# Kernel tuning notes

Measured on AMD Instinct MI355X. Metric: run time of the kernel, lower is better.

Reference implementation:

```python
import jax, jax.numpy as jnp
import numpy as np
from jax import lax

EPS = 1e-5

def conv2d(x, w, b=None, stride=1, pad=1):
    y = lax.conv_general_dilated(x, w, (stride, stride), ((pad, pad), (pad, pad)),
                                 dimension_numbers=('NCHW', 'OIHW', 'NCHW'))
    if b is not None:
        y = y + b[None, :, None, None]
    return y

def dcn(x, w_off, b_off, w, b):
    # modulated deformable conv (DCNv2): k=3, stride=1, pad=1, deformable_groups=1
    B, C, H, W = x.shape
    K = 9
    om = conv2d(x, w_off, b_off)  # [B, 3K, H, W] -> y-offsets, x-offsets, mask logits
    off_y, off_x = om[:, :K], om[:, K:2 * K]
    mask = jax.nn.sigmoid(om[:, 2 * K:])
    ky, kx = jnp.meshgrid(jnp.arange(3) - 1, jnp.arange(3) - 1, indexing='ij')
    py = jnp.arange(H)[None, None, :, None] + ky.reshape(K)[None, :, None, None] + off_y  # [B,K,H,W]
    px = jnp.arange(W)[None, None, None, :] + kx.reshape(K)[None, :, None, None] + off_x
    x_flat = x.reshape(B, C, H * W)
    y0 = jnp.floor(py)
    x0 = jnp.floor(px)
    acc = jnp.zeros((B, C, K, H * W), x.dtype)
    for dy in (0.0, 1.0):  # 4 bilinear corners (fixed small loop)
        for dx in (0.0, 1.0):
            yi = y0 + dy
            xi = x0 + dx
            wgt = (1.0 - jnp.abs(py - yi)) * (1.0 - jnp.abs(px - xi))
            valid = (yi >= 0) & (yi < H) & (xi >= 0) & (xi < W)  # zero padding outside
            yc = jnp.clip(yi, 0, H - 1).astype(jnp.int32)
            xc = jnp.clip(xi, 0, W - 1).astype(jnp.int32)
            flat = (yc * W + xc).reshape(B, K, H * W)
            g = jnp.take_along_axis(x_flat[:, :, None, :], flat[:, None, :, :], axis=3)  # [B,C,K,HW]
            acc = acc + g * (wgt * valid).reshape(B, 1, K, H * W)
    acc = acc * mask.reshape(B, 1, K, H * W)
    out = jnp.einsum('bckp,ock->bop', acc, w.reshape(w.shape[0], C, K))
    return out.reshape(B, w.shape[0], H, W) + b[None, :, None, None]

def bn_relu(x, gamma, beta, mean, var):
    inv = gamma / jnp.sqrt(var + EPS)
    return jax.nn.relu(x * inv[None, :, None, None] + (beta - mean * inv)[None, :, None, None])

def up_depthwise(x, w_up, f):
    # ConvTranspose2d(o, o, 2f, stride=f, padding=f//2, groups=o, bias=False)
    k = 2 * f
    p = k - 1 - f // 2
    return lax.conv_general_dilated(x, w_up[:, :, ::-1, ::-1], (1, 1), ((p, p), (p, p)),
                                    lhs_dilation=(f, f),
                                    dimension_numbers=('NCHW', 'OIHW', 'NCHW'),
                                    feature_group_count=w_up.shape[0])

def setup_inputs():
    key = jax.random.key(0)
    ks = jax.random.split(key, 12)
    B, CI, CO, H, W = 4, 256, 128, 64, 64
    f32 = jnp.float32
    d = {}
    d['x'] = jax.random.normal(ks[0], (B, CI, H, W), f32)
    d['w_off1'] = jax.random.normal(ks[1], (27, CI, 3, 3), f32) * 0.01
    d['b_off1'] = jnp.zeros((27,), f32)
    d['w1'] = jax.random.normal(ks[2], (CO, CI, 3, 3), f32) * (1.0 / np.sqrt(CI * 9))
    d['b1'] = jnp.zeros((CO,), f32)
    d['g1'] = jnp.ones((CO,), f32)
    d['be1'] = jnp.zeros((CO,), f32)
    d['m1'] = jax.random.normal(ks[3], (CO,), f32) * 0.1
    d['v1'] = jax.random.uniform(ks[4], (CO,), f32, 0.5, 1.5)
    d['w_up'] = jax.random.normal(ks[5], (CO, 1, 4, 4), f32) * 0.25
    d['w_off2'] = jax.random.normal(ks[6], (27, CO, 3, 3), f32) * 0.01
    d['b_off2'] = jnp.zeros((27,), f32)
    d['w2'] = jax.random.normal(ks[7], (CO, CO, 3, 3), f32) * (1.0 / np.sqrt(CO * 9))
    d['b2'] = jnp.zeros((CO,), f32)
    d['g2'] = jnp.ones((CO,), f32)
    d['be2'] = jnp.zeros((CO,), f32)
    d['m2'] = jax.random.normal(ks[8], (CO,), f32) * 0.1
    d['v2'] = jax.random.uniform(ks[9], (CO,), f32, 0.5, 1.5)
    return d

def reference(x, w_off1, b_off1, w1, b1, g1, be1, m1, v1, w_up,
              w_off2, b_off2, w2, b2, g2, be2, m2, v2):
    y = bn_relu(dcn(x, w_off1, b_off1, w1, b1), g1, be1, m1, v1)   # proj: [B,128,64,64]
    y = up_depthwise(y, w_up, 2)                                    # up:   [B,128,128,128]
    y = bn_relu(dcn(y, w_off2, b_off2, w2, b2), g2, be2, m2, v2)   # node: [B,128,128,128]
    return y
```

## Files before the change

### kernel.cpp

```cpp
#include <hip/hip_runtime.h>
#include <hip/hip_bf16.h>
#include <cmath>


#define EPSV 1e-5f

typedef __attribute__((ext_vector_type(8))) short short8;
typedef __attribute__((ext_vector_type(4))) float f32x4;

__device__ __forceinline__ ushort f2bf(float f) {
    union { float f; uint u; } v; v.f = f;
    const uint r = v.u + 0x7fffu + ((v.u >> 16) & 1u);
    return (ushort)(r >> 16);
}
__device__ __forceinline__ float bf2f(ushort h) {
    union { uint u; float f; } v; v.u = ((uint)h) << 16;
    return v.f;
}
__device__ __forceinline__ float2 ld2u(const float* p) {
    float2 v; __builtin_memcpy(&v, p, sizeof(float2)); return v;
}
__device__ __forceinline__ uint cvtpk_bf16(float a, float b) {
    uint r;
    asm("v_cvt_pk_bf16_f32 %0, %1, %2" : "=v"(r) : "v"(a), "v"(b));
    return r;
}

template <int KS>
__device__ __forceinline__ void pack_store8(
    const float* s, ushort* __restrict__ Shi, ushort* __restrict__ Slo,
    int pp, int j0)
{
    uint hw[4], lw[4];
#pragma unroll
    for (int q = 0; q < 4; ++q) {
        const float s0 = s[2 * q], s1 = s[2 * q + 1];
        const uint h = cvtpk_bf16(s0, s1);
        union { uint u; float f; } h0, h1;
        h0.u = h << 16;
        h1.u = h & 0xffff0000u;
        hw[q] = h;
        lw[q] = cvtpk_bf16(s0 - h0.f, s1 - h1.f);
    }
    uint4 hv; hv.x = hw[0]; hv.y = hw[1]; hv.z = hw[2]; hv.w = hw[3];
    uint4 lv; lv.x = lw[0]; lv.y = lw[1]; lv.z = lw[2]; lv.w = lw[3];
    *(uint4*)&Shi[pp * KS + j0] = hv;
    *(uint4*)&Slo[pp * KS + j0] = lv;
}

__global__ __launch_bounds__(256) void wsplit_perm_kernel(
    const float* __restrict__ w, ushort* __restrict__ hi,
    ushort* __restrict__ lo, int cin, int n)
{
    const int i = blockIdx.x * 256 + threadIdx.x;
    if (i >= n) return;
    const int cin9 = cin * 9;
    const int co = i / cin9;
    const int k  = i - co * cin9;
    const int ch = k >> 5;
    const int kq = (k & 31) >> 3;
    const int j  = k & 7;
    const int mt = co >> 4;
    const int lane = (co & 15) | (kq << 4);
    const size_t dst = ((size_t)(ch * 8 + mt) * 64 + lane) * 8 + j;
    const float f = w[i];
    const ushort h = f2bf(f);
    hi[dst] = h;
    lo[dst] = f2bf(f - bf2f(h));
}

__global__ __launch_bounds__(256) void wsplit_perm_conv_kernel(
    const float* __restrict__ w, ushort* __restrict__ hi,
    ushort* __restrict__ lo, int cin, int n)
{
    const int i = blockIdx.x * 256 + threadIdx.x;
    if (i >= n) return;
    const int cin9 = cin * 9;
    const int co = i / cin9;
    const int k  = i - co * cin9;
    const int ch = k >> 5;
    const int kq = (k & 31) >> 3;
    const int j  = k & 7;
    const int mt = co >> 4;
    const int lane = (co & 15) | (kq << 4);
    const size_t dst = ((size_t)(ch * 2 + mt) * 64 + lane) * 8 + j;
    const float f = (co < 27) ? w[(size_t)co * cin9 + k] : 0.f;
    const ushort h = f2bf(f);
    hi[dst] = h;
    lo[dst] = f2bf(f - bf2f(h));
}

template <int CIN, int HH, int WW, int POS, int KS>
__device__ __forceinline__ void conv_sample_chunk(
    const float* __restrict__ xb, const uint* __restrict__ toff,
    const float* __restrict__ twt, ushort* __restrict__ Shi,
    ushort* __restrict__ Slo, int tt, int kbase)
{
    constexpr int HW = HH * WW;
    const int pp = tt & (POS - 1);
    const int j0 = (tt / POS) * 8;
    float s[8];
#pragma unroll
    for (int j = 0; j < 8; ++j) {
        const int kg = kbase + j0 + j;
        const int c  = (kg * 7282) >> 16;
        const int k9 = kg - c * 9;
        const int ei = k9 * POS + pp;
        s[j] = xb[(size_t)c * HW + toff[ei]] * twt[ei];
    }
    pack_store8<KS>(s, Shi, Slo, pp, j0);
}

template <int CIN, int HH, int WW, int POS, int KWAVES, int MINW>
__global__ __launch_bounds__((POS / 16) * KWAVES * 64, MINW) void conv_mfma_kernel(
    const float* __restrict__ in,
    const ushort* __restrict__ whi,
    const ushort* __restrict__ wlo,
    const float* __restrict__ bias,
    float* __restrict__ om)
{
    constexpr int HW   = HH * WW;
    constexpr int K    = CIN * 9;
    constexpr int NPQ  = POS / 16;
    constexpr int NT   = NPQ * KWAVES * 64;
    constexpr int KC   = 32;
    constexpr int KS   = 40;
    constexpr int NCHT = K / KC;
    constexpr int NCH  = NCHT / KWAVES;
    constexpr int SBUF = POS * KS;

    extern __shared__ __align__(16) char smem[];
    uint*   toff  = (uint*)smem;
    float*  twt   = (float*)(toff + 9 * POS);
    ushort* Sbase = (ushort*)(twt + 9 * POS);

    const int tid = threadIdx.x;
    const int nt  = HW / POS;
    const int cpx = gridDim.x >> 3;
    const int bid = (blockIdx.x & 7) * cpx + (blockIdx.x >> 3);
    const int b   = bid / nt;
    const int p0  = (bid - b * nt) * POS;

    for (int i = tid; i < 9 * POS; i += NT) {
        const int k9 = i / POS, pp = i - k9 * POS;
        const int p  = p0 + pp;
        const int yy = p / WW, xx = p - yy * WW;
        const int ky = (k9 * 11) >> 5, kx = k9 - ky * 3;
        const int iy = yy + ky - 1, ix = xx + kx - 1;
        const bool v = (iy >= 0) && (iy < HH) && (ix >= 0) && (ix < WW);
        const int cy = min(max(iy, 0), HH - 1);
        const int cx = min(max(ix, 0), WW - 1);
        toff[i] = (uint)(cy * WW + cx);
        twt[i]  = v ? 1.f : 0.f;
    }
    __syncthreads();

    const float* xb = in + (size_t)b * CIN * HW;
    const int lane = tid & 63;
    const int w    = tid >> 6;
    const int wq   = w & (NPQ - 1);
    const int kgid = w / NPQ;
    const int tt   = tid & (NPQ * 64 - 1);
    ushort* S00 = Sbase + kgid * (4 * SBUF);

    f32x4 acc[2];
    acc[0] = (f32x4){0.f, 0.f, 0.f, 0.f};
    acc[1] = (f32x4){0.f, 0.f, 0.f, 0.f};
    const int mrow = lane & 15;
    const int kq   = lane >> 4;

    conv_sample_chunk<CIN, HH, WW, POS, KS>(xb, toff, twt, S00, S00 + SBUF,
                                            tt, kgid * NCH * KC);
    __syncthreads();

    for (int ch = 0; ch < NCH; ++ch) {
        const int cur = ch & 1;
        ushort* Sc = S00 + (cur * 2) * SBUF;
        const int boff = (wq * 16 + mrow) * KS + kq * 8;
        const short8 bh = *(const short8*)&Sc[boff];
        const short8 bl = *(const short8*)&Sc[SBUF + boff];
        if (ch + 1 < NCH) {
            ushort* Sn = S00 + ((cur ^ 1) * 2) * SBUF;
            conv_sample_chunk<CIN, HH, WW, POS, KS>(xb, toff, twt,
                                                    Sn, Sn + SBUF, tt,
                                                    (kgid * NCH + ch + 1) * KC);
        }
        const size_t abase = (size_t)((kgid * NCH + ch) * 2) * 512;
        __builtin_amdgcn_s_setprio(1);
#pragma unroll
        for (int mt = 0; mt < 2; ++mt) {
            const size_t ao = abase + (size_t)((mt * 64 + lane) * 8);
            const short8 ah = *(const short8*)(whi + ao);
            const short8 al = *(const short8*)(wlo + ao);
            acc[mt] = __builtin_amdgcn_mfma_f32_16x16x32_bf16(al, bh, acc[mt], 0, 0, 0);
            acc[mt] = __builtin_amdgcn_mfma_f32_16x16x32_bf16(ah, bl, acc[mt], 0, 0, 0);
            acc[mt] = __builtin_amdgcn_mfma_f32_16x16x32_bf16(ah, bh, acc[mt], 0, 0, 0);
        }
        __builtin_amdgcn_s_setprio(0);
        __syncthreads();
    }

    const int pcolb = wq * 16 + mrow;
    constexpr int RS = POS + 1;
    constexpr int SL = 32 * RS;
    float* red = (float*)Sbase;

    if constexpr (KWAVES == 4) {
        if (kgid >= 2) {
#pragma unroll
            for (int mt = 0; mt < 2; ++mt)
#pragma unroll
                for (int r = 0; r < 4; ++r) {
                    const int co = mt * 16 + kq * 4 + r;
                    red[(kgid - 2) * SL + co * RS + pcolb] = acc[mt][r];
                }
        }
        __syncthreads();
        if (kgid < 2) {
#pragma unroll
            for (int mt = 0; mt < 2; ++mt)
#pragma unroll
                for (int r = 0; r < 4; ++r) {
                    const int co = mt * 16 + kq * 4 + r;
                    acc[mt][r] += red[kgid * SL + co * RS + pcolb];
                }
        }
        __syncthreads();
        if (kgid == 1) {
#pragma unroll
            for (int mt = 0; mt < 2; ++mt)
#pragma unroll
                for (int r = 0; r < 4; ++r) {
                    const int co = mt * 16 + kq * 4 + r;
                    red[co * RS + pcolb] = acc[mt][r];
                }
        }
        __syncthreads();
        if (kgid == 0) {
#pragma unroll
            for (int mt = 0; mt < 2; ++mt)
#pragma unroll
                for (int r = 0; r < 4; ++r) {
                    const int co = mt * 16 + kq * 4 + r;
                    acc[mt][r] += red[co * RS + pcolb];
                }
        }
    } else if constexpr (KWAVES == 2) {
        if (kgid == 1) {
#pragma unroll
            for (int mt = 0; mt < 2; ++mt)
#pragma unroll
                for (int r = 0; r < 4; ++r) {
                    const int co = mt * 16 + kq * 4 + r;
                    red[co * RS + pcolb] = acc[mt][r];
                }
        }
        __syncthreads();
        if (kgid == 0) {
#pragma unroll
            for (int mt = 0; mt < 2; ++mt)
#pragma unroll
                for (int r = 0; r < 4; ++r) {
                    const int co = mt * 16 + kq * 4 + r;
                    acc[mt][r] += red[co * RS + pcolb];
                }
        }
    }

    if (kgid == 0) {
        float* ob = om + (size_t)b * 27 * HW + p0 + pcolb;
#pragma unroll
        for (int mt = 0; mt < 2; ++mt)
#pragma unroll
            for (int r = 0; r < 4; ++r) {
                const int co = mt * 16 + kq * 4 + r;
                if (co < 27)
                    ob[(size_t)co * HW] = acc[mt][r] + bias[co];
            }
    }
}

template <int CIN, int HH, int WW, int POS>
__device__ __forceinline__ void sample_issue(
    const float* __restrict__ xb, const uint* __restrict__ eoff2,
    float2* v0, float2* v1, int tt, int kbase)
{
    constexpr int HW = HH * WW;
    const int pp = tt & (POS - 1);
    const int j0 = (tt / POS) * 8;
#pragma unroll
    for (int j = 0; j < 8; ++j) {
        const int kg = kbase + j0 + j;
        const int c  = (kg * 7282) >> 16;
        const int k9 = kg - c * 9;
        const uint e = eoff2[k9 * POS + pp];
        const float* chp = xb + (size_t)c * HW;
        v0[j] = ld2u(chp + (e & 0xffffu));
        v1[j] = ld2u(chp + (e >> 16));
    }
}

template <int CIN, int HH, int WW, int POS, int KS>
__device__ __forceinline__ void sample_finish(
    const float4* __restrict__ ewt, const float2* v0, const float2* v1,
    ushort* __restrict__ Shi, ushort* __restrict__ Slo, int tt, int kbase)
{
    const int pp = tt & (POS - 1);
    const int j0 = (tt / POS) * 8;
    float s[8];
#pragma unroll
    for (int j = 0; j < 8; ++j) {
        const int kg = kbase + j0 + j;
        const int c  = (kg * 7282) >> 16;
        const int k9 = kg - c * 9;
        const float4 wv = ewt[k9 * POS + pp];
        s[j] = v0[j].x * wv.x + v0[j].y * wv.y
             + v1[j].x * wv.z + v1[j].y * wv.w;
    }
    pack_store8<KS>(s, Shi, Slo, pp, j0);
}

template <int CIN, int HH, int WW, int POS, int KS>
__device__ __forceinline__ void sample_chunk(
    const float* __restrict__ xb, const uint* __restrict__ eoff2,
    const float4* __restrict__ ewt, ushort* __restrict__ Shi,
    ushort* __restrict__ Slo, int tt, int kbase)
{
    float2 v0[8], v1[8];
    sample_issue<CIN, HH, WW, POS>(xb, eoff2, v0, v1, tt, kbase);
    sample_finish<CIN, HH, WW, POS, KS>(ewt, v0, v1, Shi, Slo, tt, kbase);
}

template <int CIN, int HH, int WW, int POS, int KWAVES, int MINW,
          bool ASTAGE, bool OMS>
__global__ __launch_bounds__((POS / 16) * KWAVES * 64, MINW) void dcn_mfma_kernel(
    const float* __restrict__ xin,
    const float* __restrict__ om,
    const float* __restrict__ omB,
    const ushort* __restrict__ whi,
    const ushort* __restrict__ wlo,
    const float* __restrict__ bias,
    const float* __restrict__ gam, const float* __restrict__ bet,
    const float* __restrict__ mu,  const float* __restrict__ var,
    float* __restrict__ out)
{
    constexpr int HW   = HH * WW;
    constexpr int K    = CIN * 9;
    constexpr int NPQ  = POS / 16;
    constexpr int NT   = NPQ * KWAVES * 64;
    constexpr int KC   = 32;
    constexpr int KS   = 40;
    constexpr int NCHT = K / KC;
    constexpr int NCH  = NCHT / KWAVES;
    constexpr int SBUF = POS * KS;
    constexpr int ABN  = ASTAGE ? 8192 : 0;
    constexpr int MTW  = 8 / NPQ;
    constexpr int NPT  = POS / 16;

    extern __shared__ __align__(16) char smem[];
    uint*    eoff2 = (uint*)smem;
    float4*  ewt   = (float4*)(eoff2 + 9 * POS);
    float*   invp  = (float*)(ewt + 9 * POS);
    float*   shp   = invp + 128;
    ushort*  Abuf  = (ushort*)(shp + 128);
    ushort*  Sbase = Abuf + ABN;

    const int tid = threadIdx.x;
    const int nt  = HW / POS;
    const int cpx = gridDim.x >> 3;
    const int bid = (blockIdx.x & 7) * cpx + (blockIdx.x >> 3);
    const int b   = bid / nt;
    const int p0  = (bid - b * nt) * POS;

    const float* omb  = om + (size_t)b * 27 * HW;
    const float* ombB = OMS ? (omB + (size_t)b * 27 * HW) : nullptr;
    for (int i = tid; i < 9 * POS; i += NT) {
        const int k9 = i / POS, pp = i - k9 * POS;
        const int p  = p0 + pp;
        const int yy = p / WW;
        const int xx = p - yy * WW;
        float oy = omb[(size_t)k9 * HW + p];
        float ox = omb[(size_t)(9 + k9) * HW + p];
        float mv = omb[(size_t)(18 + k9) * HW + p];
        if constexpr (OMS) {
            oy += ombB[(size_t)k9 * HW + p];
            ox += ombB[(size_t)(9 + k9) * HW + p];
            mv += ombB[(size_t)(18 + k9) * HW + p];
        }
        const float m  = 1.0f / (1.0f + expf(-mv));
        const int ky = (k9 * 11) >> 5;
        const int kx = k9 - ky * 3;
        const float py = (float)(yy + ky - 1) + oy;
        const float px = (float)(xx + kx - 1) + ox;
        const float y0f = floorf(py), x0f = floorf(px);
        const int   y0  = (int)y0f,  x0 = (int)x0f;
        const int by0 = min(max(y0, 0), HH - 1);
        const int by1 = min(max(y0 + 1, 0), HH - 1);
        const int bx  = min(max(x0, 0), WW - 2);
        const float wy1 = py - y0f, wx1 = px - x0f;
        const float fy0 = (y0 >= 0  && y0 < HH)     ? (1.f - wy1) * m : 0.f;
        const float fy1 = (y0 >= -1 && y0 < HH - 1) ? wy1 * m         : 0.f;
        const float fx0v = 1.f - wx1, fx1v = wx1;
        float gx0 = 0.f, gx1 = 0.f;
        if (x0 >= 0 && x0 < WW)         { if (x0 == bx)     gx0 += fx0v; else gx1 += fx0v; }
        if (x0 + 1 >= 0 && x0 + 1 < WW) { if (x0 + 1 == bx) gx0 += fx1v; else gx1 += fx1v; }
        eoff2[i] = (uint)(by0 * WW + bx) | ((uint)(by1 * WW + bx) << 16);
        float4 wv; wv.x = fy0 * gx0; wv.y = fy0 * gx1;
                   wv.z = fy1 * gx0; wv.w = fy1 * gx1;
        ewt[i] = wv;
    }
    for (int i = tid; i < 128; i += NT) {
        const float iv = gam[i] * rsqrtf(var[i] + EPSV);
        invp[i] = iv;
        shp[i]  = bet[i] - mu[i] * iv + bias[i] * iv;
    }
    __syncthreads();

    const float* xb   = xin + (size_t)b * CIN * HW;
    const int lane = tid & 63;
    const int w    = tid >> 6;
    const int wm   = w & (NPQ - 1);
    const int kgid = w / NPQ;
    const int tt   = tid & (NPQ * 64 - 1);
    const int m0   = wm * MTW;

    f32x4 acc[8];
#pragma unroll
    for (int mt = 0; mt < 8; ++mt) acc[mt] = (f32x4){0.f, 0.f, 0.f, 0.f};

    const int mrow = lane & 15;
    const int kq   = lane >> 4;

    if constexpr (ASTAGE) {
        ushort* Shi = Sbase;
        ushort* Slo = Sbase + SBUF;
        float2 v0[8], v1[8];
        sample_chunk<CIN, HH, WW, POS, KS>(xb, eoff2, ewt, Shi, Slo, tt, 0);
        {
#pragma unroll
            for (int t = 0; t < 1024 / NT; ++t) {
                const int u = tid + t * NT;
                const ushort* srcp = (u < 512)
                    ? (whi + (size_t)u * 8)
                    : (wlo + (size_t)(u - 512) * 8);
                *(short8*)&Abuf[(size_t)u * 8] = *(const short8*)srcp;
            }
        }
        if (NCH > 1)
            sample_issue<CIN, HH, WW, POS>(xb, eoff2, v0, v1, tt, KC);
        asm volatile("s_waitcnt lgkmcnt(0)" ::: "memory");
        __builtin_amdgcn_s_barrier();
        __builtin_amdgcn_sched_barrier(0);

        for (int ch = 0; ch < NCH; ++ch) {
            __builtin_amdgcn_s_setprio(1);
            short8 ahv[MTW], alv[MTW];
#pragma unroll
            for (int mt2 = 0; mt2 < MTW; ++mt2) {
                const int au = ((m0 + mt2) * 64 + lane) * 8;
                ahv[mt2] = *(const short8*)&Abuf[au];
                alv[mt2] = *(const short8*)&Abuf[4096 + au];
            }
#pragma unroll
            for (int pt = 0; pt < NPT; ++pt) {
                const int boff = (pt * 16 + mrow) * KS + kq * 8;
                const short8 bh = *(const short8*)&Shi[boff];
                const short8 bl = *(const short8*)&Slo[boff];
#pragma unroll
                for (int mt2 = 0; mt2 < MTW; ++mt2) {
                    f32x4 a = acc[mt2 * NPT + pt];
                    a = __builtin_amdgcn_mfma_f32_16x16x32_bf16(alv[mt2], bh, a, 0, 0, 0);
                    a = __builtin_amdgcn_mfma_f32_16x16x32_bf16(ahv[mt2], bl, a, 0, 0, 0);
                    a = __builtin_amdgcn_mfma_f32_16x16x32_bf16(ahv[mt2], bh, a, 0, 0, 0);
                    acc[mt2 * NPT + pt] = a;
                }
            }
            __builtin_amdgcn_s_setprio(0);
            if (ch + 1 < NCH) {
                asm volatile("s_waitcnt lgkmcnt(0)" ::: "memory");
                __builtin_amdgcn_s_barrier();
                __builtin_amdgcn_sched_barrier(0);
                const size_t wb = (size_t)(ch + 1) * 4096;
#pragma unroll
                for (int t = 0; t < 1024 / NT; ++t) {
                    const int u = tid + t * NT;
                    const ushort* srcp = (u < 512)
                        ? (whi + wb + (size_t)u * 8)
                        : (wlo + wb + (size_t)(u - 512) * 8);
                    *(short8*)&Abuf[(size_t)u * 8] = *(const short8*)srcp;
                }
                sample_finish<CIN, HH, WW, POS, KS>(ewt, v0, v1, Shi, Slo,
                                                    tt, (ch + 1) * KC);
                if (ch + 2 < NCH)
                    sample_issue<CIN, HH, WW, POS>(xb, eoff2, v0, v1, tt,
                                                   (ch + 2) * KC);
                asm volatile("s_waitcnt lgkmcnt(0)" ::: "memory");
                __builtin_amdgcn_s_barrier();
                __builtin_amdgcn_sched_barrier(0);
            }
        }
    } else {
        ushort* S00 = Sbase + kgid * (4 * SBUF);
        sample_chunk<CIN, HH, WW, POS, KS>(xb, eoff2, ewt, S00, S00 + SBUF,
                                           tt, kgid * NCH * KC);
        __syncthreads();

        for (int ch = 0; ch < NCH; ++ch) {
            const int cur = ch & 1;
            ushort* Sc = S00 + (cur * 2) * SBUF;
            short8 bhv[NPT], blv[NPT];
#pragma unroll
            for (int pt = 0; pt < NPT; ++pt) {
                const int boff = (pt * 16 + mrow) * KS + kq * 8;
                bhv[pt] = *(const short8*)&Sc[boff];
                blv[pt] = *(const short8*)&Sc[SBUF + boff];
            }
            if (ch + 1 < NCH) {
                ushort* Sn = S00 + ((cur ^ 1) * 2) * SBUF;
                sample_chunk<CIN, HH, WW, POS, KS>(xb, eoff2, ewt,
                                                   Sn, Sn + SBUF, tt,
                                                   (kgid * NCH + ch + 1) * KC);
            }
            const size_t abase = (size_t)((kgid * NCH + ch) * 8) * 512;
            __builtin_amdgcn_s_setprio(1);
#pragma unroll
            for (int mt2 = 0; mt2 < MTW; ++mt2) {
                const size_t ao = abase + (size_t)(((m0 + mt2) * 64 + lane) * 8);
                const short8 ah = *(const short8*)(whi + ao);
                const short8 al = *(const short8*)(wlo + ao);
#pragma unroll
                for (int pt = 0; pt < NPT; ++pt) {
                    f32x4 a = acc[mt2 * NPT + pt];
                    a = __builtin_amdgcn_mfma_f32_16x16x32_bf16(al, bhv[pt], a, 0, 0, 0);
                    a = __builtin_amdgcn_mfma_f32_16x16x32_bf16(ah, blv[pt], a, 0, 0, 0);
                    a = __builtin_amdgcn_mfma_f32_16x16x32_bf16(ah, bhv[pt], a, 0, 0, 0);
                    acc[mt2 * NPT + pt] = a;
                }
            }
            __builtin_amdgcn_s_setprio(0);
            __syncthreads();
        }
    }

    constexpr int RS = POS + 1;
    constexpr int SL = 128 * RS;
    float* red = (float*)Sbase;

    if constexpr (KWAVES == 4) {
        if (kgid >= 2) {
#pragma unroll
            for (int mt2 = 0; mt2 < MTW; ++mt2)
#pragma unroll
                for (int pt = 0; pt < NPT; ++pt)
#pragma unroll
                    for (int r = 0; r < 4; ++r) {
                        const int co = (m0 + mt2) * 16 + kq * 4 + r;
                        red[(kgid - 2) * SL + co * RS + pt * 16 + mrow] =
                            acc[mt2 * NPT + pt][r];
                    }
        }
        __syncthreads();
        if (kgid < 2) {
#pragma unroll
            for (int mt2 = 0; mt2 < MTW; ++mt2)
#pragma unroll
                for (int pt = 0; pt < NPT; ++pt)
#pragma unroll
                    for (int r = 0; r < 4; ++r) {
                        const int co = (m0 + mt2) * 16 + kq * 4 + r;
                        acc[mt2 * NPT + pt][r] +=
                            red[kgid * SL + co * RS + pt * 16 + mrow];
                    }
        }
        __syncthreads();
        if (kgid == 1) {
#pragma unroll
            for (int mt2 = 0; mt2 < MTW; ++mt2)
#pragma unroll
                for (int pt = 0; pt < NPT; ++pt)
#pragma unroll
                    for (int r = 0; r < 4; ++r) {
                        const int co = (m0 + mt2) * 16 + kq * 4 + r;
                        red[co * RS + pt * 16 + mrow] = acc[mt2 * NPT + pt][r];
                    }
        }
        __syncthreads();
        if (kgid == 0) {
#pragma unroll
            for (int mt2 = 0; mt2 < MTW; ++mt2)
#pragma unroll
                for (int pt = 0; pt < NPT; ++pt)
#pragma unroll
                    for (int r = 0; r < 4; ++r) {
                        const int co = (m0 + mt2) * 16 + kq * 4 + r;
                        acc[mt2 * NPT + pt][r] += red[co * RS + pt * 16 + mrow];
                    }
        }
    } else if constexpr (KWAVES == 2) {
        if (kgid == 1) {
#pragma unroll
            for (int mt2 = 0; mt2 < MTW; ++mt2)
#pragma unroll
                for (int pt = 0; pt < NPT; ++pt)
#pragma unroll
                    for (int r = 0; r < 4; ++r) {
                        const int co = (m0 + mt2) * 16 + kq * 4 + r;
                        red[co * RS + pt * 16 + mrow] = acc[mt2 * NPT + pt][r];
                    }
        }
        __syncthreads();
        if (kgid == 0) {
#pragma unroll
            for (int mt2 = 0; mt2 < MTW; ++mt2)
#pragma unroll
                for (int pt = 0; pt < NPT; ++pt)
#pragma unroll
                    for (int r = 0; r < 4; ++r) {
                        const int co = (m0 + mt2) * 16 + kq * 4 + r;
                        acc[mt2 * NPT + pt][r] += red[co * RS + pt * 16 + mrow];
                    }
        }
    }

    if (kgid == 0) {
        float* outb = out + (size_t)b * 128 * HW + p0;
#pragma unroll
        for (int mt2 = 0; mt2 < MTW; ++mt2)
#pragma unroll
            for (int pt = 0; pt < NPT; ++pt)
#pragma unroll
                for (int r = 0; r < 4; ++r) {
                    const int co = (m0 + mt2) * 16 + kq * 4 + r;
                    outb[(size_t)co * HW + pt * 16 + mrow] =
                        fmaxf(acc[mt2 * NPT + pt][r] * invp[co] + shp[co], 0.f);
                }
    }
}

__global__ __launch_bounds__(256) void upsample_kernel(
    const float* __restrict__ y,
    const float* __restrict__ wup,
    float* __restrict__ out)
{
    const int idx = blockIdx.x * 256 + threadIdx.x;
    const int ox = idx & 127;
    const int oy = (idx >> 7) & 127;
    const int c  = (idx >> 14) & 127;
    const int b  = idx >> 21;

    const float* yc = y + (size_t)(b * 128 + c) * 4096;
    const float* wc = wup + c * 16;

    float acc = 0.f;
#pragma unroll
    for (int ky = 0; ky < 4; ++ky) {
        const int qy = oy + ky - 2;
        if (qy & 1) continue;
        const int iy = qy >> 1;
        if (iy < 0 || iy >= 64) continue;
#pragma unroll
        for (int kx = 0; kx < 4; ++kx) {
            const int qx = ox + kx - 2;
            if (qx & 1) continue;
            const int ix = qx >> 1;
            if (ix < 0 || ix >= 64) continue;
            acc += yc[iy * 64 + ix] * wc[(3 - ky) * 4 + (3 - kx)];
        }
    }
    out[idx] = acc;
}

extern "C" void kernel_launch(void* const* d_in, const int* in_sizes, int n_in,
                              void* d_out, int out_size, void* d_ws, size_t ws_size,
                              hipStream_t stream) {
    const float* x      = (const float*)d_in[0];
    const float* w_off1 = (const float*)d_in[1];
    const float* b_off1 = (const float*)d_in[2];
    const float* w1     = (const float*)d_in[3];
    const float* b1     = (const float*)d_in[4];
    const float* g1v    = (const float*)d_in[5];
    const float* be1    = (const float*)d_in[6];
    const float* m1     = (const float*)d_in[7];
    const float* v1     = (const float*)d_in[8];
    const float* w_up   = (const float*)d_in[9];
    const float* w_off2 = (const float*)d_in[10];
    const float* b_off2 = (const float*)d_in[11];
    const float* w2     = (const float*)d_in[12];
    const float* b2     = (const float*)d_in[13];
    const float* g2v    = (const float*)d_in[14];
    const float* be2    = (const float*)d_in[15];
    const float* m2     = (const float*)d_in[16];
    const float* v2     = (const float*)d_in[17];

    float* ws  = (float*)d_ws;
    float* om1 = ws;
    float* y1  = om1 + 442368;
    float* up  = y1 + 2097152;
    float* om2 = up + 8388608;
    float* outf = (float*)d_out;

    ushort* w1hi  = (ushort*)up;
    ushort* w1lo  = w1hi + 294912;
    ushort* wo1hi = w1lo + 294912;
    ushort* wo1lo = wo1hi + 73728;
    ushort* w2hi  = (ushort*)y1;
    ushort* w2lo  = w2hi + 147456;
    ushort* wo2hi = w2lo + 147456;
    ushort* wo2lo = wo2hi + 36864;

    wsplit_perm_kernel<<<(294912 + 255) / 256, 256, 0, stream>>>(
        w1, w1hi, w1lo, 256, 294912);
    wsplit_perm_conv_kernel<<<(73728 + 255) / 256, 256, 0, stream>>>(
        w_off1, wo1hi, wo1lo, 256, 73728);

    conv_mfma_kernel<256, 64, 64, 16, 4, 4>
        <<<1024, 256, 21632, stream>>>(x, wo1hi, wo1lo, b_off1, om1);

    dcn_mfma_kernel<256, 64, 64, 32, 4, 4, false, false>
        <<<4 * (4096 / 32), 512, 47744, stream>>>(
        x, om1, om1, w1hi, w1lo, b1, g1v, be1, m1, v1, y1);
    upsample_kernel<<<8388608 / 256, 256, 0, stream>>>(y1, w_up, up);

    wsplit_perm_kernel<<<(147456 + 255) / 256, 256, 0, stream>>>(
        w2, w2hi, w2lo, 128, 147456);
    wsplit_perm_conv_kernel<<<(36864 + 255) / 256, 256, 0, stream>>>(
        w_off2, wo2hi, wo2lo, 128, 36864);

    conv_mfma_kernel<128, 128, 128, 64, 1, 4>
        <<<1024, 256, 25088, stream>>>(up, wo2hi, wo2lo, b_off2, om2);

    dcn_mfma_kernel<128, 128, 128, 64, 1, 4, true, false>
        <<<4 * (16384 / 64), 256, 39168, stream>>>(
        up, om2, om2, w2hi, w2lo, b2, g2v, be2, m2, v2, outf);
}
```

Measured before the change: 366.8 us.

## Deepen DCN gather prefetch to two chunks and read weights directly from global

```diff
diff --git a/kernel.cpp b/kernel.cpp
--- a/kernel.cpp
+++ b/kernel.cpp
@@ -353,7 +353,6 @@
     constexpr int NCHT = K / KC;
     constexpr int NCH  = NCHT / KWAVES;
     constexpr int SBUF = POS * KS;
-    constexpr int ABN  = ASTAGE ? 8192 : 0;
     constexpr int MTW  = 8 / NPQ;
     constexpr int NPT  = POS / 16;
 
@@ -362,8 +361,7 @@
     float4*  ewt   = (float4*)(eoff2 + 9 * POS);
     float*   invp  = (float*)(ewt + 9 * POS);
     float*   shp   = invp + 128;
-    ushort*  Abuf  = (ushort*)(shp + 128);
-    ushort*  Sbase = Abuf + ABN;
+    ushort*  Sbase = (ushort*)(shp + 128);
 
     const int tid = threadIdx.x;
     const int nt  = HW / POS;
@@ -434,69 +432,96 @@
     if constexpr (ASTAGE) {
         ushort* Shi = Sbase;
         ushort* Slo = Sbase + SBUF;
-        float2 v0[8], v1[8];
+        float2 ga0[8], ga1[8];
+        float2 gb0[8], gb1[8];
         sample_chunk<CIN, HH, WW, POS, KS>(xb, eoff2, ewt, Shi, Slo, tt, 0);
-        {
-#pragma unroll
-            for (int t = 0; t < 1024 / NT; ++t) {
-                const int u = tid + t * NT;
-                const ushort* srcp = (u < 512)
-                    ? (whi + (size_t)u * 8)
-                    : (wlo + (size_t)(u - 512) * 8);
-                *(short8*)&Abuf[(size_t)u * 8] = *(const short8*)srcp;
-            }
-        }
         if (NCH > 1)
-            sample_issue<CIN, HH, WW, POS>(xb, eoff2, v0, v1, tt, KC);
+            sample_issue<CIN, HH, WW, POS>(xb, eoff2, ga0, ga1, tt, 1 * KC);
+        if (NCH > 2)
+            sample_issue<CIN, HH, WW, POS>(xb, eoff2, gb0, gb1, tt, 2 * KC);
         asm volatile("s_waitcnt lgkmcnt(0)" ::: "memory");
         __builtin_amdgcn_s_barrier();
         __builtin_amdgcn_sched_barrier(0);
 
-        for (int ch = 0; ch < NCH; ++ch) {
-            __builtin_amdgcn_s_setprio(1);
-            short8 ahv[MTW], alv[MTW];
-#pragma unroll
-            for (int mt2 = 0; mt2 < MTW; ++mt2) {
-                const int au = ((m0 + mt2) * 64 + lane) * 8;
-                ahv[mt2] = *(const short8*)&Abuf[au];
-                alv[mt2] = *(const short8*)&Abuf[4096 + au];
+#pragma unroll 1
+        for (int ch = 0; ch < NCH; ch += 2) {
+            {
+                const size_t abase = (size_t)(ch * 8) * 512;
+                short8 ahv[MTW], alv[MTW];
+                __builtin_amdgcn_s_setprio(1);
+#pragma unroll
+                for (int mt2 = 0; mt2 < MTW; ++mt2) {
+                    const size_t ao = abase + (size_t)(((m0 + mt2) * 64 + lane) * 8);
+                    ahv[mt2] = *(const short8*)(whi + ao);
+                    alv[mt2] = *(const short8*)(wlo + ao);
+                }
+#pragma unroll
+                for (int pt = 0; pt < NPT; ++pt) {
+                    const int boff = (pt * 16 + mrow) * KS + kq * 8;
+                    const short8 bh = *(const short8*)&Shi[boff];
+                    const short8 bl = *(const short8*)&Slo[boff];
+#pragma unroll
+                    for (int mt2 = 0; mt2 < MTW; ++mt2) {
+                        f32x4 a = acc[mt2 * NPT + pt];
+                        a = __builtin_amdgcn_mfma_f32_16x16x32_bf16(alv[mt2], bh, a, 0, 0, 0);
+                        a = __builtin_amdgcn_mfma_f32_16x16x32_bf16(ahv[mt2], bl, a, 0, 0, 0);
+                        a = __builtin_amdgcn_mfma_f32_16x16x32_bf16(ahv[mt2], bh, a, 0, 0, 0);
+                        acc[mt2 * NPT + pt] = a;
+                    }
+                }
+                __builtin_amdgcn_s_setprio(0);
             }
-#pragma unroll
-            for (int pt = 0; pt < NPT; ++pt) {
-                const int boff = (pt * 16 + mrow) * KS + kq * 8;
-                const short8 bh = *(const short8*)&Shi[boff];
-                const short8 bl = *(const short8*)&Slo[boff];
-#pragma unroll
-                for (int mt2 = 0; mt2 < MTW; ++mt2) {
-                    f32x4 a = acc[mt2 * NPT + pt];
-                    a = __builtin_amdgcn_mfma_f32_16x16x32_bf16(alv[mt2], bh, a, 0, 0, 0);
-                    a = __builtin_amdgcn_mfma_f32_16x16x32_bf16(ahv[mt2], bl, a, 0, 0, 0);
-                    a = __builtin_amdgcn_mfma_f32_16x16x32_bf16(ahv[mt2], bh, a, 0, 0, 0);
-                    acc[mt2 * NPT + pt] = a;
-                }
-            }
-            __builtin_amdgcn_s_setprio(0);
             if (ch + 1 < NCH) {
                 asm volatile("s_waitcnt lgkmcnt(0)" ::: "memory");
                 __builtin_amdgcn_s_barrier();
                 __builtin_amdgcn_sched_barrier(0);
-                const size_t wb = (size_t)(ch + 1) * 4096;
-#pragma unroll
-                for (int t = 0; t < 1024 / NT; ++t) {
-                    const int u = tid + t * NT;
-                    const ushort* srcp = (u < 512)
-                        ? (whi + wb + (size_t)u * 8)
-                        : (wlo + wb + (size_t)(u - 512) * 8);
-                    *(short8*)&Abuf[(size_t)u * 8] = *(const short8*)srcp;
-                }
-                sample_finish<CIN, HH, WW, POS, KS>(ewt, v0, v1, Shi, Slo,
+                sample_finish<CIN, HH, WW, POS, KS>(ewt, ga0, ga1, Shi, Slo,
                                                     tt, (ch + 1) * KC);
-                if (ch + 2 < NCH)
-                    sample_issue<CIN, HH, WW, POS>(xb, eoff2, v0, v1, tt,
-                                                   (ch + 2) * KC);
+                if (ch + 3 < NCH)
+                    sample_issue<CIN, HH, WW, POS>(xb, eoff2, ga0, ga1, tt,
+                                                   (ch + 3) * KC);
                 asm volatile("s_waitcnt lgkmcnt(0)" ::: "memory");
                 __builtin_amdgcn_s_barrier();
                 __builtin_amdgcn_sched_barrier(0);
+                {
+                    const size_t abase = (size_t)((ch + 1) * 8) * 512;
+                    short8 ahv[MTW], alv[MTW];
+                    __builtin_amdgcn_s_setprio(1);
+#pragma unroll
+                    for (int mt2 = 0; mt2 < MTW; ++mt2) {
+                        const size_t ao = abase + (size_t)(((m0 + mt2) * 64 + lane) * 8);
+                        ahv[mt2] = *(const short8*)(whi + ao);
+                        alv[mt2] = *(const short8*)(wlo + ao);
+                    }
+#pragma unroll
+                    for (int pt = 0; pt < NPT; ++pt) {
+                        const int boff = (pt * 16 + mrow) * KS + kq * 8;
+                        const short8 bh = *(const short8*)&Shi[boff];
+                        const short8 bl = *(const short8*)&Slo[boff];
+#pragma unroll
+                        for (int mt2 = 0; mt2 < MTW; ++mt2) {
+                            f32x4 a = acc[mt2 * NPT + pt];
+                            a = __builtin_amdgcn_mfma_f32_16x16x32_bf16(alv[mt2], bh, a, 0, 0, 0);
+                            a = __builtin_amdgcn_mfma_f32_16x16x32_bf16(ahv[mt2], bl, a, 0, 0, 0);
+                            a = __builtin_amdgcn_mfma_f32_16x16x32_bf16(ahv[mt2], bh, a, 0, 0, 0);
+                            acc[mt2 * NPT + pt] = a;
+                        }
+                    }
+                    __builtin_amdgcn_s_setprio(0);
+                }
+                if (ch + 2 < NCH) {
+                    asm volatile("s_waitcnt lgkmcnt(0)" ::: "memory");
+                    __builtin_amdgcn_s_barrier();
+                    __builtin_amdgcn_sched_barrier(0);
+                    sample_finish<CIN, HH, WW, POS, KS>(ewt, gb0, gb1, Shi, Slo,
+                                                        tt, (ch + 2) * KC);
+                    if (ch + 4 < NCH)
+                        sample_issue<CIN, HH, WW, POS>(xb, eoff2, gb0, gb1, tt,
+                                                       (ch + 4) * KC);
+                    asm volatile("s_waitcnt lgkmcnt(0)" ::: "memory");
+                    __builtin_amdgcn_s_barrier();
+                    __builtin_amdgcn_sched_barrier(0);
+                }
             }
         }
     } else {
@@ -730,6 +755,6 @@
         <<<1024, 256, 25088, stream>>>(up, wo2hi, wo2lo, b_off2, om2);
 
     dcn_mfma_kernel<128, 128, 128, 64, 1, 4, true, false>
-        <<<4 * (16384 / 64), 256, 39168, stream>>>(
+        <<<4 * (16384 / 64), 256, 22784, stream>>>(
         up, om2, om2, w2hi, w2lo, b2, g2v, be2, m2, v2, outf);
 }
```

Result: slower. 405.4 us (+10.5%).
